# Performance work log

Measured on AMD Instinct MI355X. Metric: run time of the kernel, lower is better.

Reference implementation:

```python
import jax, jax.numpy as jnp
import numpy as np

B, N, F = 1024, 64, 512
EPS = 1e-8
NEG = -1e12


def setup_inputs() -> dict:
    key = jax.random.key(0)
    k1, k2, k3, k4, k5 = jax.random.split(key, 5)
    h = jax.random.normal(k1, (B, N, F), dtype=jnp.float32)
    # Linear weights stored as (in, out); math identical to torch x @ W.T
    W_h = jax.random.normal(k2, (F, F), dtype=jnp.float32) / np.sqrt(F)
    A_w1 = jax.random.normal(k3, (N, 4 * N), dtype=jnp.float32) / np.sqrt(N)
    A_w2 = jax.random.normal(k4, (4 * N, N), dtype=jnp.float32) / np.sqrt(4 * N)
    beta = jax.random.uniform(k5, (1,), dtype=jnp.float32)
    return {"h": h, "W_h": W_h, "beta": beta, "A_w1": A_w1, "A_w2": A_w2}


def _pearson_corr(x):
    # x: [B, N, F] -> pairwise Pearson correlation over feature dim: [B, N, N]
    xm = x - jnp.mean(x, axis=-1, keepdims=True)
    cov = jnp.einsum('bnf,bmf->bnm', xm, xm)          # [B, N, N]
    norm = jnp.sqrt(jnp.sum(xm * xm, axis=-1))        # [B, N]
    denom = norm[:, :, None] * norm[:, None, :] + EPS
    return cov / denom


def reference(h, W_h, beta, A_w1, A_w2):
    Wh = jnp.einsum('bnf,fg->bng', h, W_h)            # [B, N, F]
    corr_p = _pearson_corr(Wh)                        # [B, N, N]
    e = beta * jnp.abs(corr_p)                        # [B, N, N]
    # Adaptive graph structure learning: small MLP on last (node) dim
    hidden = jax.nn.relu(jnp.einsum('bnm,mk->bnk', e, A_w1))
    adj = jax.nn.relu(e + jnp.einsum('bnk,km->bnm', hidden, A_w2))
    attention = jnp.where(adj > 0, e, NEG)
    attention = jax.nn.softmax(attention, axis=-1)
    # dropout is identity in eval/reference mode
    h_prime = jnp.einsum('bnm,bmf->bnf', attention, Wh)
    return h_prime
```

## Files before the change

### kernel.cpp

```cpp
#include <hip/hip_runtime.h>
#include <math.h>

#define B_ 1024
#define N_ 64
#define F_ 512

typedef const __attribute__((address_space(1))) float* gptr_t;
typedef __attribute__((address_space(3))) float* lptr_t;
typedef _Float16 half_t;
typedef half_t half8 __attribute__((ext_vector_type(8)));
typedef half_t half4 __attribute__((ext_vector_type(4)));
typedef float f32x4 __attribute__((ext_vector_type(4)));

__device__ __forceinline__ void gload16(const float* g, float* l) {
  __builtin_amdgcn_global_load_lds((gptr_t)g, (lptr_t)l, 16, 0, 0);
}

#define XMI(n, f) ((n) * 128 + (((((f) >> 3) ^ ((n) >> 0 & 7))) << 3) + ((f) & 7))
#define SQI(n, m) ((n) * 64 + (((((m) >> 3) ^ ((n) & 7))) << 3) + ((m) & 7))

#define MFMA3(accv, ah, al, bh, bl)                                           \
  do {                                                                        \
    accv = __builtin_amdgcn_mfma_f32_16x16x32_f16(ah, bh, accv, 0, 0, 0);     \
    accv = __builtin_amdgcn_mfma_f32_16x16x32_f16(ah, bl, accv, 0, 0, 0);     \
    accv = __builtin_amdgcn_mfma_f32_16x16x32_f16(al, bh, accv, 0, 0, 0);     \
  } while (0)

__global__ __launch_bounds__(256) void k_split_w(const float* __restrict__ W,
                                                 half_t* __restrict__ wt_hi,
                                                 half_t* __restrict__ wt_lo) {
  int idx = blockIdx.x * 256 + threadIdx.x;
  int k = idx >> 9, n = idx & 511;
  float wv = W[idx] * 512.0f;
  half_t hh = (half_t)wv;
  half_t hl = (half_t)(wv - (float)hh);
  int f = (n ^ (n >> 1)) & 3;
  int pos = ((k >> 3) & 3) ^ f;
  int addr = n * 512 + (k & ~31) + (pos << 3) + (k & 7);
  wt_hi[addr] = hh;
  wt_lo[addr] = hl;
}

__global__ __launch_bounds__(256, 3) void k_wh(const float* __restrict__ hA,
                                               const half_t* __restrict__ WTh,
                                               const half_t* __restrict__ WTl,
                                               float* __restrict__ Wh) {
  __shared__ float  As[128 * 32];
  __shared__ half_t Bh[2][128 * 32];
  __shared__ half_t Bl[2][128 * 32];

  const int bid = blockIdx.x;
  const int wg  = (bid & 7) * 256 + (bid >> 3);
  const int mt  = wg >> 2;
  const int nt  = wg & 3;
  const int t = threadIdx.x;
  const int w = t >> 6, lane = t & 63;
  const int wr = w >> 1, wc = w & 1;
  const int lr = lane & 15, ko = lane >> 4;

  const float* Ab = hA + (size_t)mt * 128 * F_;
  const int n0 = nt * 128;

  int Asrc[4], Alds[4];
#pragma unroll
  for (int i = 0; i < 4; ++i) {
    int s = t + 256 * i;
    int row = s >> 3, j = s & 7;
    int jg = j ^ (row & 7);
    Asrc[i] = row * F_ + jg * 4;
    Alds[i] = s * 4;
  }
  int Bsrc[2], Blds[2];
#pragma unroll
  for (int i = 0; i < 2; ++i) {
    int s = t + 256 * i;
    int n = s >> 2, sl = s & 3;
    Bsrc[i] = (n0 + n) * 512 + sl * 8;
    Blds[i] = s * 8;
  }

  f32x4 acc[4][4];
#pragma unroll
  for (int i = 0; i < 4; ++i)
#pragma unroll
    for (int j = 0; j < 4; ++j) acc[i][j] = (f32x4){0.f, 0.f, 0.f, 0.f};

#define STAGE_A(k0)                                                          \
  do {                                                                       \
    _Pragma("unroll") for (int i_ = 0; i_ < 4; ++i_)                         \
        gload16(Ab + (size_t)(k0) + Asrc[i_], &As[Alds[i_]]);                \
  } while (0)

#define STAGE_B(buf, k0)                                                     \
  do {                                                                       \
    _Pragma("unroll") for (int i_ = 0; i_ < 2; ++i_)                         \
        gload16((const float*)(WTh + (size_t)(k0) + Bsrc[i_]),               \
                (float*)&Bh[buf][Blds[i_]]);                                 \
    _Pragma("unroll") for (int i_ = 0; i_ < 2; ++i_)                         \
        gload16((const float*)(WTl + (size_t)(k0) + Bsrc[i_]),               \
                (float*)&Bl[buf][Blds[i_]]);                                 \
  } while (0)

  STAGE_B(0, 0);
  STAGE_A(0);
  __syncthreads();

#pragma unroll 1
  for (int kt = 0; kt < 16; ++kt) {
    const int cur = kt & 1;
    if (kt < 15) STAGE_B(cur ^ 1, (kt + 1) * 32);

    half8 ah[4], al[4];
#pragma unroll
    for (int i = 0; i < 4; ++i) {
      int r = wr * 64 + i * 16 + lr;
      int p0 = (2 * ko) ^ (r & 7), p1 = (2 * ko + 1) ^ (r & 7);
      f32x4 x0 = *(const f32x4*)&As[r * 32 + p0 * 4];
      f32x4 x1 = *(const f32x4*)&As[r * 32 + p1 * 4];
#pragma unroll
      for (int q = 0; q < 4; ++q) {
        float xs = x0[q] * 16.0f;
        half_t hh = (half_t)xs;
        ah[i][q] = hh;
        al[i][q] = (half_t)(xs - (float)hh);
      }
#pragma unroll
      for (int q = 0; q < 4; ++q) {
        float xs = x1[q] * 16.0f;
        half_t hh = (half_t)xs;
        ah[i][4 + q] = hh;
        al[i][4 + q] = (half_t)(xs - (float)hh);
      }
    }

    __builtin_amdgcn_sched_barrier(0);
    __builtin_amdgcn_s_barrier();
    __builtin_amdgcn_sched_barrier(0);

    if (kt < 15) STAGE_A((kt + 1) * 32);

#pragma unroll
    for (int j = 0; j < 4; ++j) {
      int nb = wc * 64 + j * 16 + lr;
      int p = ko ^ ((nb ^ (nb >> 1)) & 3);
      half8 bh = *(const half8*)&Bh[cur][nb * 32 + p * 8];
      half8 bl = *(const half8*)&Bl[cur][nb * 32 + p * 8];
#pragma unroll
      for (int i = 0; i < 4; ++i) MFMA3(acc[i][j], ah[i], al[i], bh, bl);
    }

    __syncthreads();
  }

  const float sc = 1.0f / 8192.0f;
  float* whb = Wh + ((size_t)mt * 128 + wr * 64) * F_ + n0 + wc * 64;
#pragma unroll
  for (int i = 0; i < 4; ++i) {
#pragma unroll
    for (int rr = 0; rr < 4; ++rr) {
      int row = i * 16 + ko * 4 + rr;
#pragma unroll
      for (int j = 0; j < 4; ++j)
        whb[row * F_ + j * 16 + lr] = acc[i][j][rr] * sc;
    }
  }
#undef STAGE_A
#undef STAGE_B
}

__global__ __launch_bounds__(256) void k_attn(const float* __restrict__ Wh,
                                              const float* __restrict__ A1,
                                              const float* __restrict__ A2,
                                              const float* __restrict__ betap,
                                              float* __restrict__ out) {
  __shared__ float sm[12416];
  half_t* e_h   = (half_t*)sm;
  half_t* e_l   = e_h + 4096;
  half_t* xm_h  = (half_t*)(sm + 4096);
  half_t* xm_l  = xm_h + 8192;
  half_t* hid_h = (half_t*)(sm + 4096);
  half_t* hid_l = (half_t*)(sm + 6144);
  half_t* ab_h  = (half_t*)(sm + 8192);
  half_t* ab_l  = (half_t*)(sm + 10240);
  half_t* at_h  = (half_t*)sm;
  half_t* at_l  = at_h + 4096;
  half_t* wt_h  = (half_t*)(sm + 4096);
  half_t* wt_l  = (half_t*)(sm + 8192);
  float* mu  = sm + 12288;
  float* nrm = sm + 12352;

  const int b = blockIdx.x;
  const int t = threadIdx.x;
  const int w = t >> 6, lane = t & 63;
  const int lr = lane & 15, ko = lane >> 4;
  const float beta = betap[0];
  const float* whb = Wh + (size_t)b * N_ * F_;

  {
    int n = t >> 2, q = t & 3;
    const float* row = whb + n * F_ + q * 128;
    float s = 0.f;
#pragma unroll
    for (int i = 0; i < 32; ++i) {
      float4 v = *(const float4*)(row + i * 4);
      s += v.x + v.y + v.z + v.w;
    }
    s += __shfl_xor(s, 1);
    s += __shfl_xor(s, 2);
    if (q == 0) mu[n] = s * (1.f / F_);
  }
  __syncthreads();

  f32x4 covA[4];
#pragma unroll
  for (int j = 0; j < 4; ++j) covA[j] = (f32x4){0.f, 0.f, 0.f, 0.f};

#pragma unroll 1
  for (int c = 0; c < 4; ++c) {
#pragma unroll
    for (int i = 0; i < 8; ++i) {
      int id = t + 256 * i;
      int n = id >> 5, c4 = id & 31;
      float4 v = *(const float4*)(whb + n * F_ + c * 128 + c4 * 4);
      float m_ = mu[n];
      float x0 = (v.x - m_) * 16.f, x1 = (v.y - m_) * 16.f;
      float x2 = (v.z - m_) * 16.f, x3 = (v.w - m_) * 16.f;
      half4 hh, hl;
      hh[0] = (half_t)x0; hl[0] = (half_t)(x0 - (float)hh[0]);
      hh[1] = (half_t)x1; hl[1] = (half_t)(x1 - (float)hh[1]);
      hh[2] = (half_t)x2; hl[2] = (half_t)(x2 - (float)hh[2]);
      hh[3] = (half_t)x3; hl[3] = (half_t)(x3 - (float)hh[3]);
      int ad = n * 128 + (((c4 >> 1) ^ (n & 7)) << 3) + (c4 & 1) * 4;
      *(half4*)&xm_h[ad] = hh;
      *(half4*)&xm_l[ad] = hl;
    }
    __syncthreads();
#pragma unroll
    for (int s = 0; s < 4; ++s) {
      int ra = w * 16 + lr;
      half8 ah = *(const half8*)&xm_h[XMI(ra, (s * 4 + ko) * 8)];
      half8 al = *(const half8*)&xm_l[XMI(ra, (s * 4 + ko) * 8)];
#pragma unroll
      for (int j = 0; j < 4; ++j) {
        int rb = j * 16 + lr;
        half8 bh = *(const half8*)&xm_h[XMI(rb, (s * 4 + ko) * 8)];
        half8 bl = *(const half8*)&xm_l[XMI(rb, (s * 4 + ko) * 8)];
        covA[j] = __builtin_amdgcn_mfma_f32_16x16x32_f16(ah, bh, covA[j], 0, 0, 0);
        covA[j] = __builtin_amdgcn_mfma_f32_16x16x32_f16(ah, bl, covA[j], 0, 0, 0);
        covA[j] = __builtin_amdgcn_mfma_f32_16x16x32_f16(al, bh, covA[j], 0, 0, 0);
      }
    }
    __syncthreads();
  }

#pragma unroll
  for (int r = 0; r < 4; ++r)
    if (lr == 4 * ko + r) nrm[w * 16 + lr] = sqrtf(covA[w][r]);
  __syncthreads();

  float e32[4][4];
#pragma unroll
  for (int j = 0; j < 4; ++j) {
#pragma unroll
    for (int r = 0; r < 4; ++r) {
      int n = w * 16 + 4 * ko + r;
      int m = j * 16 + lr;
      float denom = nrm[n] * nrm[m] + 2.56e-6f;
      float e = beta * fabsf(covA[j][r] / denom);
      e32[j][r] = e;
      float es = e * 16.f;
      half_t hh = (half_t)es;
      e_h[SQI(n, m)] = hh;
      e_l[SQI(n, m)] = (half_t)(es - (float)hh);
    }
  }
  __syncthreads();

  f32x4 adj[4];
#pragma unroll
  for (int j = 0; j < 4; ++j) adj[j] = (f32x4){0.f, 0.f, 0.f, 0.f};

#pragma unroll 1
  for (int jc = 0; jc < 4; ++jc) {
#pragma unroll
    for (int hf = 0; hf < 2; ++hf) {
      int mo = w + 4 * hf;
      int jl = lane;
      half8 hh, hl;
#pragma unroll
      for (int q = 0; q < 8; ++q) {
        float x = A1[(size_t)(mo * 8 + q) * 256 + jc * 64 + jl] * 64.f;
        half_t h = (half_t)x;
        hh[q] = h; hl[q] = (half_t)(x - (float)h);
      }
      int ad = jl * 64 + ((mo ^ (jl & 7)) << 3);
      *(half8*)&ab_h[ad] = hh;
      *(half8*)&ab_l[ad] = hl;
    }
    __syncthreads();

    f32x4 h1[4];
#pragma unroll
    for (int j = 0; j < 4; ++j) h1[j] = (f32x4){0.f, 0.f, 0.f, 0.f};
#pragma unroll
    for (int s = 0; s < 2; ++s) {
      int ra = w * 16 + lr;
      half8 ah = *(const half8*)&e_h[SQI(ra, (s * 4 + ko) * 8)];
      half8 al = *(const half8*)&e_l[SQI(ra, (s * 4 + ko) * 8)];
#pragma unroll
      for (int jt = 0; jt < 4; ++jt) {
        int jl = jt * 16 + lr;
        half8 bh = *(const half8*)&ab_h[SQI(jl, (s * 4 + ko) * 8)];
        half8 bl = *(const half8*)&ab_l[SQI(jl, (s * 4 + ko) * 8)];
        h1[jt] = __builtin_amdgcn_mfma_f32_16x16x32_f16(ah, bh, h1[jt], 0, 0, 0);
        h1[jt] = __builtin_amdgcn_mfma_f32_16x16x32_f16(ah, bl, h1[jt], 0, 0, 0);
        h1[jt] = __builtin_amdgcn_mfma_f32_16x16x32_f16(al, bh, h1[jt], 0, 0, 0);
      }
    }
#pragma unroll
    for (int jt = 0; jt < 4; ++jt) {
#pragma unroll
      for (int r = 0; r < 4; ++r) {
        float x = fmaxf(h1[jt][r], 0.f);
        int n = w * 16 + 4 * ko + r;
        int jl = jt * 16 + lr;
        half_t hh = (half_t)x;
        hid_h[SQI(n, jl)] = hh;
        hid_l[SQI(n, jl)] = (half_t)(x - (float)hh);
      }
    }
    __syncthreads();

#pragma unroll
    for (int hf = 0; hf < 2; ++hf) {
      int ko2 = w + 4 * hf;
      int m = lane;
      half8 hh, hl;
#pragma unroll
      for (int q = 0; q < 8; ++q) {
        float x = A2[(size_t)(jc * 64 + ko2 * 8 + q) * 64 + m] * 64.f;
        half_t h = (half_t)x;
        hh[q] = h; hl[q] = (half_t)(x - (float)h);
      }
      int ad = m * 64 + ((ko2 ^ (m & 7)) << 3);
      *(half8*)&ab_h[ad] = hh;
      *(half8*)&ab_l[ad] = hl;
    }
    __syncthreads();

#pragma unroll
    for (int s = 0; s < 2; ++s) {
      int ra = w * 16 + lr;
      half8 ah = *(const half8*)&hid_h[SQI(ra, (s * 4 + ko) * 8)];
      half8 al = *(const half8*)&hid_l[SQI(ra, (s * 4 + ko) * 8)];
#pragma unroll
      for (int mt = 0; mt < 4; ++mt) {
        int m = mt * 16 + lr;
        half8 bh = *(const half8*)&ab_h[SQI(m, (s * 4 + ko) * 8)];
        half8 bl = *(const half8*)&ab_l[SQI(m, (s * 4 + ko) * 8)];
        adj[mt] = __builtin_amdgcn_mfma_f32_16x16x32_f16(ah, bh, adj[mt], 0, 0, 0);
        adj[mt] = __builtin_amdgcn_mfma_f32_16x16x32_f16(ah, bl, adj[mt], 0, 0, 0);
        adj[mt] = __builtin_amdgcn_mfma_f32_16x16x32_f16(al, bh, adj[mt], 0, 0, 0);
      }
    }
    __syncthreads();
  }

  {
    float p[4][4];
#pragma unroll
    for (int r = 0; r < 4; ++r) {
      float mx = -3.0e38f;
#pragma unroll
      for (int mt = 0; mt < 4; ++mt) {
        float pre = e32[mt][r] + adj[mt][r] * (1.f / 65536.f);
        p[mt][r] = (pre > 0.f) ? e32[mt][r] : -1e12f;
        mx = fmaxf(mx, p[mt][r]);
      }
      mx = fmaxf(mx, __shfl_xor(mx, 1));
      mx = fmaxf(mx, __shfl_xor(mx, 2));
      mx = fmaxf(mx, __shfl_xor(mx, 4));
      mx = fmaxf(mx, __shfl_xor(mx, 8));
      float ssum = 0.f;
#pragma unroll
      for (int mt = 0; mt < 4; ++mt) {
        p[mt][r] = expf(p[mt][r] - mx);
        ssum += p[mt][r];
      }
      ssum += __shfl_xor(ssum, 1);
      ssum += __shfl_xor(ssum, 2);
      ssum += __shfl_xor(ssum, 4);
      ssum += __shfl_xor(ssum, 8);
      float inv = 1.f / ssum;
      int n = w * 16 + 4 * ko + r;
#pragma unroll
      for (int mt = 0; mt < 4; ++mt) {
        float pv = p[mt][r] * inv;
        int m = mt * 16 + lr;
        half_t hh = (half_t)pv;
        at_h[SQI(n, m)] = hh;
        at_l[SQI(n, m)] = (half_t)(pv - (float)hh);
      }
    }
  }

  const int fl0 = t & 127;
  const int moB = t >> 7;
#pragma unroll 1
  for (int fc = 0; fc < 4; ++fc) {
    __syncthreads();
#pragma unroll
    for (int i = 0; i < 4; ++i) {
      int mo = moB + 2 * i;
      half8 hh, hl;
#pragma unroll
      for (int q = 0; q < 8; ++q) {
        float x = whb[(size_t)(mo * 8 + q) * F_ + fc * 128 + fl0];
        half_t h = (half_t)x;
        hh[q] = h; hl[q] = (half_t)(x - (float)h);
      }
      int ad = fl0 * 64 + ((mo ^ (fl0 & 7)) << 3);
      *(half8*)&wt_h[ad] = hh;
      *(half8*)&wt_l[ad] = hl;
    }
    __syncthreads();

    half8 aah[2], aal[2];
#pragma unroll
    for (int s = 0; s < 2; ++s) {
      int n = w * 16 + lr;
      aah[s] = *(const half8*)&at_h[SQI(n, (s * 4 + ko) * 8)];
      aal[s] = *(const half8*)&at_l[SQI(n, (s * 4 + ko) * 8)];
    }
#pragma unroll
    for (int ft = 0; ft < 8; ++ft) {
      f32x4 po = (f32x4){0.f, 0.f, 0.f, 0.f};
#pragma unroll
      for (int s = 0; s < 2; ++s) {
        int fl = ft * 16 + lr;
        int ad = fl * 64 + (((((s * 4 + ko)) ^ (fl & 7))) << 3);
        half8 bh = *(const half8*)&wt_h[ad];
        half8 bl = *(const half8*)&wt_l[ad];
        po = __builtin_amdgcn_mfma_f32_16x16x32_f16(aah[s], bh, po, 0, 0, 0);
        po = __builtin_amdgcn_mfma_f32_16x16x32_f16(aah[s], bl, po, 0, 0, 0);
        po = __builtin_amdgcn_mfma_f32_16x16x32_f16(aal[s], bh, po, 0, 0, 0);
      }
      int fg = fc * 128 + ft * 16 + lr;
#pragma unroll
      for (int r = 0; r < 4; ++r) {
        int n = w * 16 + 4 * ko + r;
        out[(size_t)b * N_ * F_ + n * F_ + fg] = po[r];
      }
    }
  }
}

extern "C" void kernel_launch(void* const* d_in, const int* in_sizes, int n_in,
                              void* d_out, int out_size, void* d_ws, size_t ws_size,
                              hipStream_t stream) {
  const float* h    = (const float*)d_in[0];
  const float* W    = (const float*)d_in[1];
  const float* beta = (const float*)d_in[2];
  const float* A1   = (const float*)d_in[3];
  const float* A2   = (const float*)d_in[4];
  float* out = (float*)d_out;
  float* Wh  = (float*)d_ws;

  half_t* wt_hi = (half_t*)d_out;
  half_t* wt_lo = wt_hi + 512 * 512;

  k_split_w<<<1024, 256, 0, stream>>>(W, wt_hi, wt_lo);
  k_wh<<<2048, 256, 0, stream>>>(h, wt_hi, wt_lo, Wh);
  k_attn<<<B_, 256, 0, stream>>>(Wh, A1, A2, beta, out);
}
```

Measured before the change: 261.3 us.

## Prefetch next chunk's global loads into registers before MFMA compute

In the fused attention kernel, the per-chunk global loads (centered Wh tiles, A1/A2 weight slices, and Wh transposed tiles) now go into register buffers one stage ahead. Each load is issued right after the LDS write barrier, so global latency overlaps the MFMA work on the current chunk. This raises register pressure (up to 32 extra floats live), which could lower occupancy.

Result: faster. 222.4 us (-14.9%).

```diff
diff --git a/kernel.cpp b/kernel.cpp
--- a/kernel.cpp
+++ b/kernel.cpp
@@ -196,6 +196,16 @@
   const float beta = betap[0];
   const float* whb = Wh + (size_t)b * N_ * F_;
 
+  float4 vbuf[8];
+#define LOAD_XM(c_)                                                           \
+  do {                                                                        \
+    _Pragma("unroll") for (int i_ = 0; i_ < 8; ++i_) {                        \
+      int id_ = t + 256 * i_;                                                 \
+      int n_ = id_ >> 5, c4_ = id_ & 31;                                      \
+      vbuf[i_] = *(const float4*)(whb + n_ * F_ + (c_) * 128 + c4_ * 4);      \
+    }                                                                         \
+  } while (0)
+
   {
     int n = t >> 2, q = t & 3;
     const float* row = whb + n * F_ + q * 128;
@@ -209,6 +219,7 @@
     s += __shfl_xor(s, 2);
     if (q == 0) mu[n] = s * (1.f / F_);
   }
+  LOAD_XM(0);
   __syncthreads();
 
   f32x4 covA[4];
@@ -221,7 +232,7 @@
     for (int i = 0; i < 8; ++i) {
       int id = t + 256 * i;
       int n = id >> 5, c4 = id & 31;
-      float4 v = *(const float4*)(whb + n * F_ + c * 128 + c4 * 4);
+      float4 v = vbuf[i];
       float m_ = mu[n];
       float x0 = (v.x - m_) * 16.f, x1 = (v.y - m_) * 16.f;
       float x2 = (v.z - m_) * 16.f, x3 = (v.w - m_) * 16.f;
@@ -235,6 +246,7 @@
       *(half4*)&xm_l[ad] = hl;
     }
     __syncthreads();
+    if (c < 3) LOAD_XM(c + 1);
 #pragma unroll
     for (int s = 0; s < 4; ++s) {
       int ra = w * 16 + lr;
@@ -252,6 +264,7 @@
     }
     __syncthreads();
   }
+#undef LOAD_XM
 
 #pragma unroll
   for (int r = 0; r < 4; ++r)
@@ -274,6 +287,24 @@
       e_l[SQI(n, m)] = (half_t)(es - (float)hh);
     }
   }
+
+  float a1buf[16], a2buf[16];
+#define LOAD_A1(jc_)                                                          \
+  do {                                                                        \
+    _Pragma("unroll") for (int hf_ = 0; hf_ < 2; ++hf_)                       \
+      _Pragma("unroll") for (int q_ = 0; q_ < 8; ++q_)                        \
+        a1buf[hf_ * 8 + q_] =                                                 \
+            A1[(size_t)((w + 4 * hf_) * 8 + q_) * 256 + (jc_) * 64 + lane];   \
+  } while (0)
+#define LOAD_A2(jc_)                                                          \
+  do {                                                                        \
+    _Pragma("unroll") for (int hf_ = 0; hf_ < 2; ++hf_)                       \
+      _Pragma("unroll") for (int q_ = 0; q_ < 8; ++q_)                        \
+        a2buf[hf_ * 8 + q_] =                                                 \
+            A2[(size_t)((jc_) * 64 + (w + 4 * hf_) * 8 + q_) * 64 + lane];    \
+  } while (0)
+
+  LOAD_A1(0);
   __syncthreads();
 
   f32x4 adj[4];
@@ -289,7 +320,7 @@
       half8 hh, hl;
 #pragma unroll
       for (int q = 0; q < 8; ++q) {
-        float x = A1[(size_t)(mo * 8 + q) * 256 + jc * 64 + jl] * 64.f;
+        float x = a1buf[hf * 8 + q] * 64.f;
         half_t h = (half_t)x;
         hh[q] = h; hl[q] = (half_t)(x - (float)h);
       }
@@ -298,6 +329,7 @@
       *(half8*)&ab_l[ad] = hl;
     }
     __syncthreads();
+    LOAD_A2(jc);
 
     f32x4 h1[4];
 #pragma unroll
@@ -338,7 +370,7 @@
       half8 hh, hl;
 #pragma unroll
       for (int q = 0; q < 8; ++q) {
-        float x = A2[(size_t)(jc * 64 + ko2 * 8 + q) * 64 + m] * 64.f;
+        float x = a2buf[hf * 8 + q] * 64.f;
         half_t h = (half_t)x;
         hh[q] = h; hl[q] = (half_t)(x - (float)h);
       }
@@ -347,6 +379,7 @@
       *(half8*)&ab_l[ad] = hl;
     }
     __syncthreads();
+    if (jc < 3) LOAD_A1(jc + 1);
 
 #pragma unroll
     for (int s = 0; s < 2; ++s) {
@@ -365,6 +398,8 @@
     }
     __syncthreads();
   }
+#undef LOAD_A1
+#undef LOAD_A2
 
   {
     float p[4][4];
@@ -406,6 +441,18 @@
 
   const int fl0 = t & 127;
   const int moB = t >> 7;
+  float wbuf[32];
+#define LOAD_WT(fc_)                                                          \
+  do {                                                                        \
+    _Pragma("unroll") for (int i_ = 0; i_ < 4; ++i_) {                        \
+      int mo_ = moB + 2 * i_;                                                 \
+      _Pragma("unroll") for (int q_ = 0; q_ < 8; ++q_)                        \
+        wbuf[i_ * 8 + q_] =                                                   \
+            whb[(size_t)(mo_ * 8 + q_) * F_ + (fc_) * 128 + fl0];             \
+    }                                                                         \
+  } while (0)
+
+  LOAD_WT(0);
 #pragma unroll 1
   for (int fc = 0; fc < 4; ++fc) {
     __syncthreads();
@@ -415,7 +462,7 @@
       half8 hh, hl;
 #pragma unroll
       for (int q = 0; q < 8; ++q) {
-        float x = whb[(size_t)(mo * 8 + q) * F_ + fc * 128 + fl0];
+        float x = wbuf[i * 8 + q];
         half_t h = (half_t)x;
         hh[q] = h; hl[q] = (half_t)(x - (float)h);
       }
@@ -424,6 +471,7 @@
       *(half8*)&wt_l[ad] = hl;
     }
     __syncthreads();
+    if (fc < 3) LOAD_WT(fc + 1);
 
     half8 aah[2], aal[2];
 #pragma unroll
@@ -453,6 +501,7 @@
       }
     }
   }
+#undef LOAD_WT
 }
 
 extern "C" void kernel_launch(void* const* d_in, const int* in_sizes, int n_in,
```
